# Performance work log

Measured on AMD Instinct MI355X. Metric: run time of the kernel, lower is better.

The kernel has to match this reference:

```python
import jax, jax.numpy as jnp
import numpy as np
from jax import lax

NPOINT = 1024
NSAMPLES = (16, 32, 64)
BN_EPS = 1e-5


def fps(xyz, npoint):
    """Farthest point sampling. xyz: [B,N,3] -> idx [B,npoint].
    Deterministic start at index 0 (torch version uses a random start)."""
    B, N, _ = xyz.shape

    def step(carry, _):
        dist, far = carry
        centroid = jnp.take_along_axis(xyz, far[:, None, None], axis=1)  # [B,1,3]
        d = jnp.sum((xyz - centroid) ** 2, axis=-1)                      # [B,N]
        dist = jnp.minimum(dist, d)
        nxt = jnp.argmax(dist, axis=1)
        return (dist, nxt), far

    init = (jnp.full((B, N), 1e10, xyz.dtype), jnp.zeros((B,), jnp.int32))
    _, idxs = lax.scan(step, init, None, length=npoint)  # [npoint,B]
    return idxs.T


def gather_points(points, idx):
    # points [B,N,C], idx [B,...] -> [B,...,C]
    return jax.vmap(lambda p, i: p[i])(points, idx)


def sq_cdist(a, b):
    # a [B,S,3], b [B,N,3] -> squared distances [B,S,N] (same ordering as cdist)
    aa = jnp.sum(a * a, -1)[:, :, None]
    bb = jnp.sum(b * b, -1)[:, None, :]
    return aa + bb - 2.0 * jnp.einsum('bsc,bnc->bsn', a, b)


def mlp_scale(g, ws, gs, bs):
    # g: [B,S,k,Cin]; 1x1 conv + BatchNorm (training-mode stats) + ReLU per layer
    for w, gm, bt in zip(ws, gs, bs):
        g = jnp.einsum('bskc,oc->bsko', g, w)
        mu = jnp.mean(g, axis=(0, 1, 2))
        var = jnp.var(g, axis=(0, 1, 2))
        g = jax.nn.relu((g - mu) * lax.rsqrt(var + BN_EPS) * gm + bt)
    return g


def setup_inputs() -> dict:
    key = jax.random.key(0)
    ks = jax.random.split(key, 16)
    B, N, C = 16, 4096, 64
    xyz = jax.random.normal(ks[0], (B, N, 3), jnp.float32)
    features = jax.random.normal(ks[1], (B, N, C), jnp.float32)
    # stacked per-scale MLP params; layer dims: 67 -> 64 -> 64 -> 128
    w0 = jax.random.normal(ks[2], (3, 64, 67), jnp.float32) * 0.1
    w1 = jax.random.normal(ks[3], (3, 64, 64), jnp.float32) * 0.1
    w2 = jax.random.normal(ks[4], (3, 128, 64), jnp.float32) * 0.1
    g0 = jnp.ones((3, 64), jnp.float32); b0 = jnp.zeros((3, 64), jnp.float32)
    g1 = jnp.ones((3, 64), jnp.float32); b1 = jnp.zeros((3, 64), jnp.float32)
    g2 = jnp.ones((3, 128), jnp.float32); b2 = jnp.zeros((3, 128), jnp.float32)
    return {"xyz": xyz, "features": features, "w0": w0, "w1": w1, "w2": w2,
            "g0": g0, "g1": g1, "g2": g2, "b0": b0, "b1": b1, "b2": b2}


def reference(xyz, features, w0, w1, w2, g0, g1, g2, b0, b1, b2):
    fps_idx = fps(xyz, NPOINT)                                   # [B,S]
    new_xyz = jnp.take_along_axis(xyz, fps_idx[..., None], axis=1)  # [B,S,3]
    d2 = sq_cdist(new_xyz, xyz)                                  # [B,S,N]
    outs = []
    for s, nsample in enumerate(NSAMPLES):
        _, idx = lax.top_k(-d2, nsample)                         # k nearest, [B,S,k]
        grouped_xyz = gather_points(xyz, idx) - new_xyz[:, :, None, :]
        grouped_f = gather_points(features, idx)
        g = jnp.concatenate([grouped_xyz, grouped_f], axis=-1)   # [B,S,k,67]
        g = mlp_scale(g, (w0[s], w1[s], w2[s]), (g0[s], g1[s], g2[s]), (b0[s], b1[s], b2[s]))
        outs.append(jnp.max(g, axis=2))                          # max over neighbors -> [B,S,128]
    fused = jnp.concatenate(outs, axis=-1)                       # [B,S,384]
    return new_xyz, fused
```

## Files before the change

### kernel.cpp

```cpp
#include <hip/hip_runtime.h>
#include <stdint.h>

#define BATCH 16
#define NPTS  4096
#define NSAMP 1024

typedef __attribute__((ext_vector_type(8))) short  short8;
typedef __attribute__((ext_vector_type(4))) float  floatx4;

__device__ __forceinline__ unsigned short f2bf(float f) {
    unsigned u = __float_as_uint(f);
    unsigned r = (u + 0x7FFFu + ((u >> 16) & 1u)) >> 16;
    return (unsigned short)r;
}

template<int CTRL>
__device__ __forceinline__ uint64_t dpp_max_u64(uint64_t k) {
    int lo = (int)(unsigned)k;
    int hi = (int)(unsigned)(k >> 32);
    int lo2 = __builtin_amdgcn_update_dpp(0, lo, CTRL, 0xF, 0xF, false);
    int hi2 = __builtin_amdgcn_update_dpp(0, hi, CTRL, 0xF, 0xF, false);
    uint64_t o = ((uint64_t)(unsigned)hi2 << 32) | (unsigned)lo2;
    return o > k ? o : k;
}

__global__ __launch_bounds__(512) void fps_conv_kernel(
    const float* __restrict__ xyz,
    float* __restrict__ out_xyz,
    const float* __restrict__ feat,
    unsigned short* __restrict__ featb,
    int staged)
{
#pragma clang fp contract(off)
    if (blockIdx.x >= 16) {
        if (staged) {
            int t = (blockIdx.x - 16) * 512 + threadIdx.x;
            const float4* fp = (const float4*)feat + (size_t)t*2;
            float4 a = fp[0], c = fp[1];
            uint4 o;
            o.x = (unsigned)f2bf(a.x) | ((unsigned)f2bf(a.y) << 16);
            o.y = (unsigned)f2bf(a.z) | ((unsigned)f2bf(a.w) << 16);
            o.z = (unsigned)f2bf(c.x) | ((unsigned)f2bf(c.y) << 16);
            o.w = (unsigned)f2bf(c.z) | ((unsigned)f2bf(c.w) << 16);
            ((uint4*)featb)[t] = o;
        }
        return;
    }

    const int b    = blockIdx.x;
    const int tid  = threadIdx.x;
    const int lane = tid & 63;
    const int wave = tid >> 6;
    const float* xb = xyz + (size_t)b * NPTS * 3;

    __shared__ float xsh[NPTS], ysh[NPTS], zsh[NPTS];
    __shared__ float cents[NSAMP * 3];
    __shared__ uint64_t keylds[2][8];

    float px[8], py[8], pz[8], dist[8];
    unsigned nidx[8];
#pragma unroll
    for (int i = 0; i < 8; ++i) {
        int p = tid + (i << 9);
        px[i] = xb[p*3+0];
        py[i] = xb[p*3+1];
        pz[i] = xb[p*3+2];
        dist[i] = 1e10f;
        nidx[i] = ~(unsigned)p;
        xsh[p] = px[i]; ysh[p] = py[i]; zsh[p] = pz[i];
    }
    __syncthreads();

    float cx = xb[0], cy = xb[1], cz = xb[2];

    for (int it = 0; it < NSAMP; ++it) {
        if (tid == 0) {
            cents[it*3+0] = cx; cents[it*3+1] = cy; cents[it*3+2] = cz;
        }
        if (it == NSAMP - 1) break;

        uint64_t k[8];
#pragma unroll
        for (int i = 0; i < 8; ++i) {
            float dx = px[i] - cx, dy = py[i] - cy, dz = pz[i] - cz;
            float d = dx*dx; d = d + dy*dy; d = d + dz*dz;
            float nd = fminf(dist[i], d);
            dist[i] = nd;
            k[i] = ((uint64_t)__float_as_uint(nd) << 32) | nidx[i];
        }
        uint64_t m0 = k[0] > k[1] ? k[0] : k[1];
        uint64_t m1 = k[2] > k[3] ? k[2] : k[3];
        uint64_t m2 = k[4] > k[5] ? k[4] : k[5];
        uint64_t m3 = k[6] > k[7] ? k[6] : k[7];
        uint64_t ma = m0 > m1 ? m0 : m1;
        uint64_t mb = m2 > m3 ? m2 : m3;
        uint64_t kk = ma > mb ? ma : mb;

        kk = dpp_max_u64<0x121>(kk);
        kk = dpp_max_u64<0x122>(kk);
        kk = dpp_max_u64<0x124>(kk);
        kk = dpp_max_u64<0x128>(kk);
        kk = dpp_max_u64<0x142>(kk);
        kk = dpp_max_u64<0x143>(kk);

        int pb = it & 1;
        if (lane == 63) keylds[pb][wave] = kk;
        __syncthreads();

        uint64_t f = keylds[pb][lane & 7];
        f = dpp_max_u64<0x121>(f);
        f = dpp_max_u64<0x122>(f);
        f = dpp_max_u64<0x124>(f);
        int cur = (int)~((unsigned)f);

        cx = xsh[cur]; cy = ysh[cur]; cz = zsh[cur];
    }

    __syncthreads();
    for (int i = tid; i < NSAMP*3; i += 512)
        out_xyz[(size_t)b*NSAMP*3 + i] = cents[i];
}

#define WT_S 18432

__global__ __launch_bounds__(256) void conv_w_kernel(
    const float* __restrict__ w0, const float* __restrict__ w1,
    const float* __restrict__ w2, unsigned short* __restrict__ wtab)
{
    int t = blockIdx.x * 256 + threadIdx.x;
    if (t >= 3*WT_S) return;
    int s = t / WT_S, r = t % WT_S;
    unsigned short v = 0;
    if (r < 6144) {
        int n = r / 96, kg = r % 96;
        if (kg < 67) {
            int ci = (kg < 64) ? (kg + 3) : (kg - 64);
            v = f2bf(w0[(size_t)(s*64 + n)*67 + ci]);
        }
    } else if (r < 10240) {
        int idx = r - 6144;
        v = f2bf(w1[(size_t)(s*64 + (idx >> 6))*64 + (idx & 63)]);
    } else {
        int idx = r - 10240;
        v = f2bf(w2[(size_t)(s*128 + (idx >> 6))*64 + (idx & 63)]);
    }
    wtab[t] = v;
}

__global__ __launch_bounds__(256) void knn_kernel(
    const float* __restrict__ xyz,
    const float* __restrict__ new_xyz,
    unsigned short* __restrict__ knn_idx)
{
#pragma clang fp contract(off)
    __shared__ float xs[NPTS], ys[NPTS], zs[NPTS];
    __shared__ uint64_t buf[4][64];
    const int tid  = threadIdx.x;
    const int lane = tid & 63;
    const int wave = tid >> 6;
    const int q = blockIdx.x * 4 + wave;
    const int b = q >> 10;
    const float* xb = xyz + (size_t)b * NPTS * 3;

    for (int i = tid; i < NPTS; i += 256) {
        xs[i] = xb[i*3+0];
        ys[i] = xb[i*3+1];
        zs[i] = xb[i*3+2];
    }
    __syncthreads();

    const float qx = new_xyz[q*3+0], qy = new_xyz[q*3+1], qz = new_xyz[q*3+2];
    float aa = qx*qx; aa = aa + qy*qy; aa = aa + qz*qz;

    auto keyof = [&](int c) -> unsigned {
        float x = xs[c], y = ys[c], z = zs[c];
        float bb = x*x;  bb = bb + y*y;   bb = bb + z*z;
        float dt = qx*x; dt = dt + qy*y;  dt = dt + qz*z;
        float d2 = (aa + bb) - 2.0f*dt;
        unsigned u = __float_as_uint(d2);
        return (u & 0x80000000u) ? ~u : (u | 0x80000000u);
    };
    auto shfl64 = [&](uint64_t v, int src) -> uint64_t {
        int lo = __shfl((int)(unsigned)v, src);
        int hi = __shfl((int)(unsigned)(v >> 32), src);
        return ((uint64_t)(unsigned)hi << 32) | (unsigned)lo;
    };
    auto shflx64 = [&](uint64_t v, int m) -> uint64_t {
        int lo = __shfl_xor((int)(unsigned)v, m);
        int hi = __shfl_xor((int)(unsigned)(v >> 32), m);
        return ((uint64_t)(unsigned)hi << 32) | (unsigned)lo;
    };
    auto sortP = [&](uint64_t &p) {
#pragma unroll
        for (int kk = 2; kk <= 64; kk <<= 1) {
#pragma unroll
            for (int j = kk >> 1; j >= 1; j >>= 1) {
                uint64_t o = shflx64(p, j);
                bool up    = ((lane & kk) == 0);
                bool lower = ((lane & j) == 0);
                bool oless = o < p;
                bool keep  = (up == lower) ? oless : !oless;
                if (keep) p = o;
            }
        }
    };
    auto mergeP = [&](uint64_t &P, uint64_t Bv) {
        uint64_t rev = shfl64(Bv, 63 - lane);
        if (rev < P) P = rev;
#pragma unroll
        for (int j = 32; j >= 1; j >>= 1) {
            uint64_t o = shflx64(P, j);
            bool lower = ((lane & j) == 0);
            bool oless = o < P;
            bool keep  = lower ? oless : !oless;
            if (keep) P = o;
        }
    };

    uint64_t P = ((uint64_t)keyof(lane) << 32) | (unsigned)lane;
    sortP(P);
    uint64_t Pmax = shfl64(P, 63);
    int cnt = 0;

    for (int bt = 1; bt < 64; ++bt) {
        int c = (bt << 6) + lane;
        uint64_t cand = ((uint64_t)keyof(c) << 32) | (unsigned)c;
        bool qual = cand < Pmax;
        unsigned long long mask = __ballot(qual);
        if (mask == 0ull) continue;
        int n = __popcll(mask);
        if (cnt + n > 64) {
            uint64_t Bv = (lane < cnt) ? buf[wave][lane] : ~0ull;
            sortP(Bv);
            mergeP(P, Bv);
            Pmax = shfl64(P, 63);
            cnt = 0;
            qual = qual && (cand < Pmax);
            mask = __ballot(qual);
            n = __popcll(mask);
        }
        if (qual) {
            int pos = cnt + __popcll(mask & ((1ull << lane) - 1ull));
            buf[wave][pos] = cand;
        }
        cnt += n;
    }
    if (cnt > 0) {
        uint64_t Bv = (lane < cnt) ? buf[wave][lane] : ~0ull;
        sortP(Bv);
        mergeP(P, Bv);
    }
    knn_idx[(size_t)q*64 + lane] = (unsigned short)(P & 0xFFFFu);
}

#define GPB 8

template<int PHASE>
__global__ __launch_bounds__(256) void mlp_phase(
    const float* __restrict__ xyz,
    const float* __restrict__ feat,
    const float* __restrict__ new_xyz,
    const unsigned short* __restrict__ knn,
    const unsigned short* __restrict__ featb,
    int staged,
    const unsigned short* __restrict__ wtab,
    const float* __restrict__ bnp,
    float* __restrict__ stats,
    float* __restrict__ out1)
{
    __shared__ __align__(16) unsigned short g_lds[64*104];
    __shared__ __align__(16) unsigned short a_lds[64*72];
    __shared__ float stat_lds[256];
    __shared__ float wavemax[4*128];

    const int tid  = threadIdx.x;
    const int lane = tid & 63;
    const int wave = tid >> 6;
    const int n16  = lane & 15;
    const int quad = lane >> 4;

    int scale, g0;
    {
        int xcd = blockIdx.x & 7;
        int r   = blockIdx.x >> 3;
        int hi  = (r >= 224) ? 1 : 0;
        int bt  = 2*xcd + hi;
        int r2  = r - hi*224;
        if (r2 < 32)       { scale = 0; g0 = bt*256  + r2*GPB; }
        else if (r2 < 96)  { scale = 1; g0 = bt*512  + (r2-32)*GPB; }
        else               { scale = 2; g0 = bt*1024 + (r2-96)*GPB; }
    }
    const int KNB = 16 << scale;
    const int cpg = 4 >> scale;
    const int wpc = 1 << scale;

    const unsigned short* wt  = wtab + scale * WT_S;
    const unsigned short* w2b = wt + 6144;
    const unsigned short* w3b = wt + 10240;

    short8 w1f[4][3];
#pragma unroll
    for (int nt = 0; nt < 4; ++nt)
#pragma unroll
        for (int kb = 0; kb < 3; ++kb)
            w1f[nt][kb] = *(const short8*)&wt[(nt*16 + n16)*96 + kb*32 + quad*8];

    float s1p[4], t1p[4], s2p[4], t2p[4];
    if constexpr (PHASE >= 2) {
#pragma unroll
        for (int nt = 0; nt < 4; ++nt) {
            int o = ((0*3 + scale)*128 + nt*16 + n16)*2;
            s1p[nt] = bnp[o]; t1p[nt] = bnp[o+1];
        }
    }
    if constexpr (PHASE >= 3) {
#pragma unroll
        for (int nt = 0; nt < 4; ++nt) {
            int o = ((1*3 + scale)*128 + nt*16 + n16)*2;
            s2p[nt] = bnp[o]; t2p[nt] = bnp[o+1];
        }
    }

    float sac[8], sqac[8];
#pragma unroll
    for (int i = 0; i < 8; ++i) { sac[i] = 0.f; sqac[i] = 0.f; }
    stat_lds[tid] = 0.f;
    {
        const int r = tid >> 2;
        const int sub = tid & 3;
        if (sub == 0)      *(uint4*)&g_lds[r*104 + 72] = make_uint4(0u,0u,0u,0u);
        else if (sub == 1) *(uint4*)&g_lds[r*104 + 80] = make_uint4(0u,0u,0u,0u);
        else if (sub == 2) *(uint4*)&g_lds[r*104 + 88] = make_uint4(0u,0u,0u,0u);
    }
    __syncthreads();

    for (int g = g0; g < g0 + GPB; ++g) {
        const int cb = g * cpg;
        {
            const int r   = tid >> 2;
            const int sub = tid & 3;
            const int ci  = cb + (r >> (4 + scale));
            const int j   = r & (KNB - 1);
            const int n   = knn[(size_t)ci*64 + j];
            const int b   = ci >> 10;
            if (staged) {
                const unsigned short* frow = featb + ((size_t)(b*NPTS + n))*64 + sub*16;
                uint4 c0 = ((const uint4*)frow)[0];
                uint4 c1 = ((const uint4*)frow)[1];
                *(uint4*)&g_lds[r*104 + sub*16]     = c0;
                *(uint4*)&g_lds[r*104 + sub*16 + 8] = c1;
            } else {
                const float* frow = feat + ((size_t)(b*NPTS + n))*64 + sub*16;
                unsigned short h[16];
#pragma unroll
                for (int u = 0; u < 16; ++u) h[u] = f2bf(frow[u]);
                uint4 p0, p1;
                p0.x = (unsigned)h[0]  | ((unsigned)h[1]  << 16);
                p0.y = (unsigned)h[2]  | ((unsigned)h[3]  << 16);
                p0.z = (unsigned)h[4]  | ((unsigned)h[5]  << 16);
                p0.w = (unsigned)h[6]  | ((unsigned)h[7]  << 16);
                p1.x = (unsigned)h[8]  | ((unsigned)h[9]  << 16);
                p1.y = (unsigned)h[10] | ((unsigned)h[11] << 16);
                p1.z = (unsigned)h[12] | ((unsigned)h[13] << 16);
                p1.w = (unsigned)h[14] | ((unsigned)h[15] << 16);
                *(uint4*)&g_lds[r*104 + sub*16]     = p0;
                *(uint4*)&g_lds[r*104 + sub*16 + 8] = p1;
            }
            if (sub == 0) {
                const float* nx = new_xyz + (size_t)ci*3;
                const float* xp = xyz + ((size_t)(b*NPTS + n))*3;
                unsigned short h0 = f2bf(xp[0] - nx[0]);
                unsigned short h1 = f2bf(xp[1] - nx[1]);
                unsigned short h2 = f2bf(xp[2] - nx[2]);
                uint4 z = make_uint4((unsigned)h0 | ((unsigned)h1 << 16),
                                     (unsigned)h2, 0u, 0u);
                *(uint4*)&g_lds[r*104 + 64] = z;
            }
        }
        __syncthreads();

        const int rb = wave*16 + n16;
        short8 a0 = *(const short8*)&g_lds[rb*104 +      quad*8];
        short8 a1 = *(const short8*)&g_lds[rb*104 + 32 + quad*8];
        short8 a2 = *(const short8*)&g_lds[rb*104 + 64 + quad*8];
        floatx4 acc[4];
#pragma unroll
        for (int nt = 0; nt < 4; ++nt) {
            floatx4 c = {0.f,0.f,0.f,0.f};
            c = __builtin_amdgcn_mfma_f32_16x16x32_bf16(a0, w1f[nt][0], c, 0,0,0);
            c = __builtin_amdgcn_mfma_f32_16x16x32_bf16(a1, w1f[nt][1], c, 0,0,0);
            c = __builtin_amdgcn_mfma_f32_16x16x32_bf16(a2, w1f[nt][2], c, 0,0,0);
            acc[nt] = c;
        }

        if constexpr (PHASE == 1) {
#pragma unroll
            for (int nt = 0; nt < 4; ++nt) {
                floatx4 c = acc[nt];
                sac[nt]  += c[0]+c[1]+c[2]+c[3];
                sqac[nt] += c[0]*c[0]+c[1]*c[1]+c[2]*c[2]+c[3]*c[3];
            }
        }
        if constexpr (PHASE >= 2) {
#pragma unroll
            for (int nt = 0; nt < 4; ++nt) {
                int ch = nt*16 + n16;
#pragma unroll
                for (int r = 0; r < 4; ++r) {
                    float v = acc[nt][r]*s1p[nt] + t1p[nt];
                    v = fmaxf(v, 0.f);
                    a_lds[(wave*16 + quad*4 + r)*72 + ch] = f2bf(v);
                }
            }
            short8 e0 = *(const short8*)&a_lds[rb*72 +      quad*8];
            short8 e1 = *(const short8*)&a_lds[rb*72 + 32 + quad*8];
            floatx4 acc2[4];
#pragma unroll
            for (int nt = 0; nt < 4; ++nt) {
                short8 wa = *(const short8*)&w2b[(nt*16 + n16)*64 +      quad*8];
                short8 wb = *(const short8*)&w2b[(nt*16 + n16)*64 + 32 + quad*8];
                floatx4 c = {0.f,0.f,0.f,0.f};
                c = __builtin_amdgcn_mfma_f32_16x16x32_bf16(e0, wa, c, 0,0,0);
                c = __builtin_amdgcn_mfma_f32_16x16x32_bf16(e1, wb, c, 0,0,0);
                acc2[nt] = c;
            }
            if constexpr (PHASE == 2) {
#pragma unroll
                for (int nt = 0; nt < 4; ++nt) {
                    floatx4 c = acc2[nt];
                    sac[nt]  += c[0]+c[1]+c[2]+c[3];
                    sqac[nt] += c[0]*c[0]+c[1]*c[1]+c[2]*c[2]+c[3]*c[3];
                }
            }
            if constexpr (PHASE == 3) {
#pragma unroll
                for (int nt = 0; nt < 4; ++nt) {
                    int ch = nt*16 + n16;
#pragma unroll
                    for (int r = 0; r < 4; ++r) {
                        float v = acc2[nt][r]*s2p[nt] + t2p[nt];
                        v = fmaxf(v, 0.f);
                        a_lds[(wave*16 + quad*4 + r)*72 + ch] = f2bf(v);
                    }
                }
                short8 f0 = *(const short8*)&a_lds[rb*72 +      quad*8];
                short8 f1 = *(const short8*)&a_lds[rb*72 + 32 + quad*8];
#pragma unroll
                for (int nt = 0; nt < 8; ++nt) {
                    short8 wa = *(const short8*)&w3b[(nt*16 + n16)*64 +      quad*8];
                    short8 wb = *(const short8*)&w3b[(nt*16 + n16)*64 + 32 + quad*8];
                    floatx4 c = {0.f,0.f,0.f,0.f};
                    c = __builtin_amdgcn_mfma_f32_16x16x32_bf16(f0, wa, c, 0,0,0);
                    c = __builtin_amdgcn_mfma_f32_16x16x32_bf16(f1, wb, c, 0,0,0);
                    sac[nt]  += c[0]+c[1]+c[2]+c[3];
                    sqac[nt] += c[0]*c[0]+c[1]*c[1]+c[2]*c[2]+c[3]*c[3];
                    float m = fmaxf(fmaxf(c[0],c[1]), fmaxf(c[2],c[3]));
                    m = fmaxf(m, __shfl_xor(m, 16));
                    m = fmaxf(m, __shfl_xor(m, 32));
                    if (lane < 16) wavemax[wave*128 + nt*16 + n16] = m;
                }
            }
        }
        __syncthreads();
        if constexpr (PHASE == 3) {
            const int ch = tid & 127;
            for (int ic = tid >> 7; ic < cpg; ic += 2) {
                float m = wavemax[(ic*wpc)*128 + ch];
                for (int w = 1; w < wpc; ++w)
                    m = fmaxf(m, wavemax[(ic*wpc + w)*128 + ch]);
                out1[(size_t)(cb + ic)*384 + scale*128 + ch] = m;
            }
        }
    }

    const int NCH = (PHASE == 3) ? 8 : 4;
#pragma unroll
    for (int nt = 0; nt < 8; ++nt) {
        if (nt >= NCH) break;
        float v  = sac[nt], v2 = sqac[nt];
        v  += __shfl_xor(v, 16);  v  += __shfl_xor(v, 32);
        v2 += __shfl_xor(v2, 16); v2 += __shfl_xor(v2, 32);
        if (lane < 16) {
            int ch = nt*16 + n16;
            atomicAdd(&stat_lds[ch*2],   v);
            atomicAdd(&stat_lds[ch*2+1], v2);
        }
    }
    __syncthreads();
    const int layer = PHASE - 1;
    const int nch = (PHASE == 3) ? 128 : 64;
    if (tid < nch*2) {
        atomicAdd(&stats[(size_t)(layer*3 + scale)*256 + tid], stat_lds[tid]);
    }
}

__global__ void bn_params_kernel(
    const float* __restrict__ stats, float* __restrict__ bnp,
    const float* __restrict__ gamma, const float* __restrict__ beta,
    int layer, int nch)
{
    int t = blockIdx.x * blockDim.x + threadIdx.x;
    if (t >= 3*nch) return;
    int scale = t / nch, ch = t % nch;
    float M = 16384.0f * (float)(16 << scale);
    int o = ((layer*3 + scale)*128 + ch)*2;
    float sum = stats[o], sumsq = stats[o+1];
    float mean = sum / M;
    float var = sumsq / M - mean*mean;
    var = fmaxf(var, 0.f);
    float ga = gamma[scale*nch + ch];
    float be = beta[scale*nch + ch];
    float s  = ga / sqrtf(var + 1e-5f);
    float tt = be - mean * s;
    bnp[o] = s; bnp[o+1] = tt;
}

__global__ void finalize_kernel(
    const float* __restrict__ bnp,
    float* __restrict__ out1)
{
    int t = blockIdx.x * 256 + threadIdx.x;
    float4 m = ((const float4*)out1)[t];
    int c0 = (t*4) % 384;
    int scale = c0 >> 7;
    int ch = c0 & 127;
    int o = ((2*3 + scale)*128 + ch)*2;
    float4 r;
    r.x = fmaxf(m.x*bnp[o+0] + bnp[o+1], 0.f);
    r.y = fmaxf(m.y*bnp[o+2] + bnp[o+3], 0.f);
    r.z = fmaxf(m.z*bnp[o+4] + bnp[o+5], 0.f);
    r.w = fmaxf(m.w*bnp[o+6] + bnp[o+7], 0.f);
    ((float4*)out1)[t] = r;
}

extern "C" void kernel_launch(void* const* d_in, const int* in_sizes, int n_in,
                              void* d_out, int out_size, void* d_ws, size_t ws_size,
                              hipStream_t stream)
{
    (void)in_sizes; (void)n_in; (void)out_size;
    const float* xyz  = (const float*)d_in[0];
    const float* feat = (const float*)d_in[1];
    const float* w0   = (const float*)d_in[2];
    const float* w1   = (const float*)d_in[3];
    const float* w2   = (const float*)d_in[4];
    const float* g0   = (const float*)d_in[5];
    const float* g1   = (const float*)d_in[6];
    const float* g2   = (const float*)d_in[7];
    const float* b0   = (const float*)d_in[8];
    const float* b1   = (const float*)d_in[9];
    const float* b2   = (const float*)d_in[10];
    float* out  = (float*)d_out;
    float* out0 = out;
    float* out1 = out + 49152;

    char* ws = (char*)d_ws;
    const size_t NEED_FULL = 2097152ull + 8388608ull + 9216 + 9216 + 110592;
    const int staged = (ws_size >= NEED_FULL) ? 1 : 0;
    unsigned short* knn   = (unsigned short*)ws;
    unsigned short* featb = staged ? (unsigned short*)(ws + 2097152) : nullptr;
    size_t tail = staged ? (2097152ull + 8388608ull) : 2097152ull;
    float* stats = (float*)(ws + tail);
    float* bnp   = (float*)(ws + tail + 9216);
    unsigned short* wtab = (unsigned short*)(ws + tail + 18432);

    hipMemsetAsync(stats, 0, 9216, stream);
    fps_conv_kernel<<<16 + (staged ? 1024 : 0), 512, 0, stream>>>(
        xyz, out0, feat, featb, staged);
    conv_w_kernel<<<216, 256, 0, stream>>>(w0, w1, w2, wtab);
    knn_kernel<<<4096, 256, 0, stream>>>(xyz, out0, knn);

    mlp_phase<1><<<3584,256,0,stream>>>(xyz,feat,out0,knn,featb,staged,wtab,bnp,stats,out1);
    bn_params_kernel<<<1,256,0,stream>>>(stats, bnp, g0, b0, 0, 64);

    mlp_phase<2><<<3584,256,0,stream>>>(xyz,feat,out0,knn,featb,staged,wtab,bnp,stats,out1);
    bn_params_kernel<<<1,256,0,stream>>>(stats, bnp, g1, b1, 1, 64);

    mlp_phase<3><<<3584,256,0,stream>>>(xyz,feat,out0,knn,featb,staged,wtab,bnp,stats,out1);
    bn_params_kernel<<<2,256,0,stream>>>(stats, bnp, g2, b2, 2, 128);

    finalize_kernel<<<6144, 256, 0, stream>>>(bnp, out1);
}
```

Baseline: 1.352 ms.

## Double-buffer neighbor gather in MLP phases and widen KNN blocks to 8 waves

The MLP phase kernels now use two LDS gather buffers. The next group's neighbor features and relative coordinates are loaded into registers before the current group's MFMA work and written to the other buffer afterward, so gather latency overlaps compute and one barrier per iteration is removed. The wavemax buffer is also double-buffered so the PHASE 3 max read does not race with the next iteration's writes. Separately, the KNN kernel runs 8 query waves per 512-thread block instead of 4, so the per-batch point cloud staged into LDS is shared by twice as many queries. The cost is higher register pressure from the in-flight prefetch and more LDS per block, which may lower occupancy.

Measured after the change: 1.455 ms. 1.08x slower.

```diff
diff --git a/kernel.cpp b/kernel.cpp
--- a/kernel.cpp
+++ b/kernel.cpp
@@ -147,22 +147,22 @@
     wtab[t] = v;
 }
 
-__global__ __launch_bounds__(256) void knn_kernel(
+__global__ __launch_bounds__(512) void knn_kernel(
     const float* __restrict__ xyz,
     const float* __restrict__ new_xyz,
     unsigned short* __restrict__ knn_idx)
 {
 #pragma clang fp contract(off)
     __shared__ float xs[NPTS], ys[NPTS], zs[NPTS];
-    __shared__ uint64_t buf[4][64];
+    __shared__ uint64_t buf[8][64];
     const int tid  = threadIdx.x;
     const int lane = tid & 63;
     const int wave = tid >> 6;
-    const int q = blockIdx.x * 4 + wave;
+    const int q = blockIdx.x * 8 + wave;
     const int b = q >> 10;
     const float* xb = xyz + (size_t)b * NPTS * 3;
 
-    for (int i = tid; i < NPTS; i += 256) {
+    for (int i = tid; i < NPTS; i += 512) {
         xs[i] = xb[i*3+0];
         ys[i] = xb[i*3+1];
         zs[i] = xb[i*3+2];
@@ -268,16 +268,18 @@
     float* __restrict__ stats,
     float* __restrict__ out1)
 {
-    __shared__ __align__(16) unsigned short g_lds[64*104];
+    __shared__ __align__(16) unsigned short g_lds[2][64*104];
     __shared__ __align__(16) unsigned short a_lds[64*72];
     __shared__ float stat_lds[256];
-    __shared__ float wavemax[4*128];
+    __shared__ float wavemax[2][4*128];
 
     const int tid  = threadIdx.x;
     const int lane = tid & 63;
     const int wave = tid >> 6;
     const int n16  = lane & 15;
     const int quad = lane >> 4;
+    const int gr_r   = tid >> 2;
+    const int gr_sub = tid & 3;
 
     int scale, g0;
     {
@@ -325,64 +327,70 @@
 #pragma unroll
     for (int i = 0; i < 8; ++i) { sac[i] = 0.f; sqac[i] = 0.f; }
     stat_lds[tid] = 0.f;
-    {
-        const int r = tid >> 2;
-        const int sub = tid & 3;
-        if (sub == 0)      *(uint4*)&g_lds[r*104 + 72] = make_uint4(0u,0u,0u,0u);
-        else if (sub == 1) *(uint4*)&g_lds[r*104 + 80] = make_uint4(0u,0u,0u,0u);
-        else if (sub == 2) *(uint4*)&g_lds[r*104 + 88] = make_uint4(0u,0u,0u,0u);
-    }
+#pragma unroll
+    for (int bb = 0; bb < 2; ++bb) {
+        if (gr_sub == 0)      *(uint4*)&g_lds[bb][gr_r*104 + 72] = make_uint4(0u,0u,0u,0u);
+        else if (gr_sub == 1) *(uint4*)&g_lds[bb][gr_r*104 + 80] = make_uint4(0u,0u,0u,0u);
+        else if (gr_sub == 2) *(uint4*)&g_lds[bb][gr_r*104 + 88] = make_uint4(0u,0u,0u,0u);
+    }
+
+    auto stage_load = [&](int gq, uint4& c0, uint4& c1, uint4& z) {
+        const int cb2 = gq * cpg;
+        const int ci  = cb2 + (gr_r >> (4 + scale));
+        const int j   = gr_r & (KNB - 1);
+        const int n   = knn[(size_t)ci*64 + j];
+        const int b   = ci >> 10;
+        if (staged) {
+            const unsigned short* frow = featb + ((size_t)(b*NPTS + n))*64 + gr_sub*16;
+            c0 = ((const uint4*)frow)[0];
+            c1 = ((const uint4*)frow)[1];
+        } else {
+            const float* frow = feat + ((size_t)(b*NPTS + n))*64 + gr_sub*16;
+            unsigned short h[16];
+#pragma unroll
+            for (int u = 0; u < 16; ++u) h[u] = f2bf(frow[u]);
+            c0.x = (unsigned)h[0]  | ((unsigned)h[1]  << 16);
+            c0.y = (unsigned)h[2]  | ((unsigned)h[3]  << 16);
+            c0.z = (unsigned)h[4]  | ((unsigned)h[5]  << 16);
+            c0.w = (unsigned)h[6]  | ((unsigned)h[7]  << 16);
+            c1.x = (unsigned)h[8]  | ((unsigned)h[9]  << 16);
+            c1.y = (unsigned)h[10] | ((unsigned)h[11] << 16);
+            c1.z = (unsigned)h[12] | ((unsigned)h[13] << 16);
+            c1.w = (unsigned)h[14] | ((unsigned)h[15] << 16);
+        }
+        if (gr_sub == 0) {
+            const float* nx = new_xyz + (size_t)ci*3;
+            const float* xp = xyz + ((size_t)(b*NPTS + n))*3;
+            unsigned short h0 = f2bf(xp[0] - nx[0]);
+            unsigned short h1 = f2bf(xp[1] - nx[1]);
+            unsigned short h2 = f2bf(xp[2] - nx[2]);
+            z = make_uint4((unsigned)h0 | ((unsigned)h1 << 16),
+                           (unsigned)h2, 0u, 0u);
+        }
+    };
+    auto stage_write = [&](int bb, const uint4& c0, const uint4& c1,
+                           const uint4& z) {
+        *(uint4*)&g_lds[bb][gr_r*104 + gr_sub*16]     = c0;
+        *(uint4*)&g_lds[bb][gr_r*104 + gr_sub*16 + 8] = c1;
+        if (gr_sub == 0) *(uint4*)&g_lds[bb][gr_r*104 + 64] = z;
+    };
+
+    uint4 sc0, sc1, sz;
+    stage_load(g0, sc0, sc1, sz);
+    stage_write(0, sc0, sc1, sz);
     __syncthreads();
 
     for (int g = g0; g < g0 + GPB; ++g) {
-        const int cb = g * cpg;
-        {
-            const int r   = tid >> 2;
-            const int sub = tid & 3;
-            const int ci  = cb + (r >> (4 + scale));
-            const int j   = r & (KNB - 1);
-            const int n   = knn[(size_t)ci*64 + j];
-            const int b   = ci >> 10;
-            if (staged) {
-                const unsigned short* frow = featb + ((size_t)(b*NPTS + n))*64 + sub*16;
-                uint4 c0 = ((const uint4*)frow)[0];
-                uint4 c1 = ((const uint4*)frow)[1];
-                *(uint4*)&g_lds[r*104 + sub*16]     = c0;
-                *(uint4*)&g_lds[r*104 + sub*16 + 8] = c1;
-            } else {
-                const float* frow = feat + ((size_t)(b*NPTS + n))*64 + sub*16;
-                unsigned short h[16];
-#pragma unroll
-                for (int u = 0; u < 16; ++u) h[u] = f2bf(frow[u]);
-                uint4 p0, p1;
-                p0.x = (unsigned)h[0]  | ((unsigned)h[1]  << 16);
-                p0.y = (unsigned)h[2]  | ((unsigned)h[3]  << 16);
-                p0.z = (unsigned)h[4]  | ((unsigned)h[5]  << 16);
-                p0.w = (unsigned)h[6]  | ((unsigned)h[7]  << 16);
-                p1.x = (unsigned)h[8]  | ((unsigned)h[9]  << 16);
-                p1.y = (unsigned)h[10] | ((unsigned)h[11] << 16);
-                p1.z = (unsigned)h[12] | ((unsigned)h[13] << 16);
-                p1.w = (unsigned)h[14] | ((unsigned)h[15] << 16);
-                *(uint4*)&g_lds[r*104 + sub*16]     = p0;
-                *(uint4*)&g_lds[r*104 + sub*16 + 8] = p1;
-            }
-            if (sub == 0) {
-                const float* nx = new_xyz + (size_t)ci*3;
-                const float* xp = xyz + ((size_t)(b*NPTS + n))*3;
-                unsigned short h0 = f2bf(xp[0] - nx[0]);
-                unsigned short h1 = f2bf(xp[1] - nx[1]);
-                unsigned short h2 = f2bf(xp[2] - nx[2]);
-                uint4 z = make_uint4((unsigned)h0 | ((unsigned)h1 << 16),
-                                     (unsigned)h2, 0u, 0u);
-                *(uint4*)&g_lds[r*104 + 64] = z;
-            }
-        }
-        __syncthreads();
+        const int cur = (g - g0) & 1;
+        const int cb  = g * cpg;
+        const bool more = (g + 1 < g0 + GPB);
+        if (more) stage_load(g + 1, sc0, sc1, sz);
 
         const int rb = wave*16 + n16;
-        short8 a0 = *(const short8*)&g_lds[rb*104 +      quad*8];
-        short8 a1 = *(const short8*)&g_lds[rb*104 + 32 + quad*8];
-        short8 a2 = *(const short8*)&g_lds[rb*104 + 64 + quad*8];
+        const unsigned short* gb = g_lds[cur];
+        short8 a0 = *(const short8*)&gb[rb*104 +      quad*8];
+        short8 a1 = *(const short8*)&gb[rb*104 + 32 + quad*8];
+        short8 a2 = *(const short8*)&gb[rb*104 + 64 + quad*8];
         floatx4 acc[4];
 #pragma unroll
         for (int nt = 0; nt < 4; ++nt) {
@@ -457,17 +465,19 @@
                     float m = fmaxf(fmaxf(c[0],c[1]), fmaxf(c[2],c[3]));
                     m = fmaxf(m, __shfl_xor(m, 16));
                     m = fmaxf(m, __shfl_xor(m, 32));
-                    if (lane < 16) wavemax[wave*128 + nt*16 + n16] = m;
+                    if (lane < 16) wavemax[cur][wave*128 + nt*16 + n16] = m;
                 }
             }
         }
+
+        if (more) stage_write(cur ^ 1, sc0, sc1, sz);
         __syncthreads();
         if constexpr (PHASE == 3) {
             const int ch = tid & 127;
             for (int ic = tid >> 7; ic < cpg; ic += 2) {
-                float m = wavemax[(ic*wpc)*128 + ch];
+                float m = wavemax[cur][(ic*wpc)*128 + ch];
                 for (int w = 1; w < wpc; ++w)
-                    m = fmaxf(m, wavemax[(ic*wpc + w)*128 + ch]);
+                    m = fmaxf(m, wavemax[cur][(ic*wpc + w)*128 + ch]);
                 out1[(size_t)(cb + ic)*384 + scale*128 + ch] = m;
             }
         }
@@ -567,7 +577,7 @@
     fps_conv_kernel<<<16 + (staged ? 1024 : 0), 512, 0, stream>>>(
         xyz, out0, feat, featb, staged);
     conv_w_kernel<<<216, 256, 0, stream>>>(w0, w1, w2, wtab);
-    knn_kernel<<<4096, 256, 0, stream>>>(xyz, out0, knn);
+    knn_kernel<<<2048, 512, 0, stream>>>(xyz, out0, knn);
 
     mlp_phase<1><<<3584,256,0,stream>>>(xyz,feat,out0,knn,featb,staged,wtab,bnp,stats,out1);
     bn_params_kernel<<<1,256,0,stream>>>(stats, bnp, g0, b0, 0, 64);
```
